# Kernel optimization log

Measured on AMD Instinct MI355X. Metric: run time of the kernel, lower is better.

The kernel has to match this reference:

```python
import jax, jax.numpy as jnp
import numpy as np

B, HID, REC, NC, T = 512, 196, 488, 35, 120
BN_EPS = 1e-3


def _bn(x, g, b):
    # eval-mode CustomBatchNorm1d: running_mean=0, running_var=1
    return g * (x / jnp.sqrt(1.0 + BN_EPS)) + b


def _gru(x, Wih, Whh, bih, bhh):
    """Standard torch nn.GRU (batch_first), h0 = 0. x: [B,T,D] -> [B,T,H]."""
    H = Whh.shape[1]
    def step(h, xt):
        xg = xt @ Wih.T + bih          # [B,3H]
        hg = h @ Whh.T + bhh           # [B,3H]
        xr, xz, xn = jnp.split(xg, 3, axis=1)
        hr, hz, hn = jnp.split(hg, 3, axis=1)
        r = jax.nn.sigmoid(xr + hr)
        z = jax.nn.sigmoid(xz + hz)
        n = jnp.tanh(xn + r * hn)
        h2 = (1.0 - z) * n + z * h
        return h2, h2
    h0 = jnp.zeros((x.shape[0], H), x.dtype)
    _, ys = jax.lax.scan(step, h0, jnp.swapaxes(x, 0, 1))
    return jnp.swapaxes(ys, 0, 1)


def _custom_gru(x, Wih, Whh, bih):
    """CustomGRUCell (eval mode: prev_target=0 so weight_tf term vanishes)."""
    H = Whh.shape[1]
    Whh_rz = Whh[:2 * H]
    Whh_n = Whh[2 * H:]
    b_r, b_z, b_n = bih[:H], bih[H:2 * H], bih[2 * H:]
    def step(h, xt):
        xg = xt @ Wih.T                 # [B,3H], no bias in F.linear
        xr, xz, xn = jnp.split(xg, 3, axis=1)
        hg = h @ Whh_rz.T               # only r,z rows needed (h_h chunk unused)
        hr, hz = jnp.split(hg, 2, axis=1)
        r = jax.nn.sigmoid(xr + hr + b_r)
        u = jax.nn.sigmoid(xz + hz + b_z)
        n = jax.nn.softmax(xn + (r * h) @ Whh_n.T + b_n, axis=1)
        h2 = (1.0 - u) * n + u * h
        return h2, h2
    h0 = jnp.zeros((x.shape[0], H), x.dtype)
    _, ys = jax.lax.scan(step, h0, jnp.swapaxes(x, 0, 1))
    return jnp.swapaxes(ys, 0, 1)


def setup_inputs() -> dict:
    key = jax.random.key(0)
    ks = jax.random.split(key, 16)
    s = 0.05
    inp = {
        "z_in": jax.random.normal(ks[0], (B, HID), jnp.float32),
        "W0": jax.random.normal(ks[1], (HID, HID), jnp.float32) * s,
        "b0": jnp.zeros((HID,), jnp.float32),
        "g0": jnp.full((1, HID), 0.1, jnp.float32),
        "beta0": jnp.zeros((1, HID), jnp.float32),
        "W1": jax.random.normal(ks[2], (HID, HID), jnp.float32) * s,
        "b1": jnp.zeros((HID,), jnp.float32),
        "g1": jnp.full((1, HID), 0.1, jnp.float32),
        "beta1": jnp.zeros((1, HID), jnp.float32),
        "gru0_Wih": jax.random.normal(ks[3], (3 * REC, HID), jnp.float32) * s,
        "gru0_Whh": jax.random.normal(ks[4], (3 * REC, REC), jnp.float32) * s,
        "gru0_bih": jax.random.normal(ks[5], (3 * REC,), jnp.float32) * s,
        "gru0_bhh": jax.random.normal(ks[6], (3 * REC,), jnp.float32) * s,
        "gru1_Wih": jax.random.normal(ks[7], (3 * REC, REC), jnp.float32) * s,
        "gru1_Whh": jax.random.normal(ks[8], (3 * REC, REC), jnp.float32) * s,
        "gru1_bih": jax.random.normal(ks[9], (3 * REC,), jnp.float32) * s,
        "gru1_bhh": jax.random.normal(ks[10], (3 * REC,), jnp.float32) * s,
        "cell_Wih": jax.random.normal(ks[11], (3 * NC, REC), jnp.float32) * s,
        "cell_Whh": jax.random.normal(ks[12], (3 * NC, NC), jnp.float32) * s,
        "cell_bih": jax.random.normal(ks[13], (3 * NC,), jnp.float32) * s,
    }
    return inp


def reference(z_in, W0, b0, g0, beta0, W1, b1, g1, beta1,
              gru0_Wih, gru0_Whh, gru0_bih, gru0_bhh,
              gru1_Wih, gru1_Whh, gru1_bih, gru1_bhh,
              cell_Wih, cell_Whh, cell_bih):
    z = _bn(z_in @ W0.T + b0, g0, beta0)
    z = _bn(z @ W1.T + b1, g1, beta1)
    z_reps = jnp.broadcast_to(z[:, None, :], (z.shape[0], T, z.shape[1]))
    x = _gru(z_reps, gru0_Wih, gru0_Whh, gru0_bih, gru0_bhh)
    x = _gru(x, gru1_Wih, gru1_Whh, gru1_bih, gru1_bhh)
    x_out = _custom_gru(x, cell_Wih, cell_Whh, cell_bih)  # [B,T,NCHARS]
    return x_out
```

## Files before the change

### kernel.cpp

```cpp
#include <hip/hip_runtime.h>
#include <math.h>

#define Bsz 512
#define HID 196
#define REC 488
#define NC  35
#define TT  120
#define G3  (3*REC)

#define KT   16
#define NT   31
#define AS   36
#define WS   36

struct GSmem   { float A[2][KT][AS]; float W[2][3][KT][WS]; };
struct CellSmem{ float xs[4][492]; float hs[4][40]; float rh[4][40]; };
union  PipeSmem{ GSmem g; CellSmem c; };

__device__ __forceinline__ float sigmoidf_(float x) { return 1.0f / (1.0f + __expf(-x)); }

__global__ void dense_bn_kernel(const float* __restrict__ X, const float* __restrict__ W,
                                const float* __restrict__ bias, const float* __restrict__ g,
                                const float* __restrict__ beta, float* __restrict__ Y) {
  __shared__ float xs[HID];
  int b = blockIdx.x;
  for (int k = threadIdx.x; k < HID; k += blockDim.x) xs[k] = X[(size_t)b*HID + k];
  __syncthreads();
  int j = threadIdx.x;
  if (j < HID) {
    const float4* wr = (const float4*)(W + (size_t)j*HID);
    float acc = 0.f;
    #pragma unroll 7
    for (int k4 = 0; k4 < HID/4; ++k4) {
      float4 w4 = wr[k4];
      acc += xs[4*k4+0]*w4.x + xs[4*k4+1]*w4.y + xs[4*k4+2]*w4.z + xs[4*k4+3]*w4.w;
    }
    float v = (acc + bias[j]) * 0.9995003746f;
    Y[(size_t)b*HID + j] = g[j]*v + beta[j];
  }
}

__global__ void xg0_kernel(const float* __restrict__ Z, const float* __restrict__ Wih,
                           const float* __restrict__ bih, float* __restrict__ XG) {
  __shared__ float zs[HID];
  int b = blockIdx.x;
  for (int k = threadIdx.x; k < HID; k += blockDim.x) zs[k] = Z[(size_t)b*HID + k];
  __syncthreads();
  for (int c = threadIdx.x; c < G3; c += blockDim.x) {
    const float4* wr = (const float4*)(Wih + (size_t)c*HID);
    float acc = 0.f;
    for (int k4 = 0; k4 < HID/4; ++k4) {
      float4 w4 = wr[k4];
      acc += zs[4*k4+0]*w4.x + zs[4*k4+1]*w4.y + zs[4*k4+2]*w4.z + zs[4*k4+3]*w4.w;
    }
    XG[(size_t)b*G3 + c] = acc + bih[c];
  }
}

__device__ __forceinline__ void loadA32(float (&dst)[KT][AS], const float* __restrict__ A,
                                        int b0, int kk) {
  int t = threadIdx.x;
  if (t < 128) {
    int row  = t >> 2;
    int kloc = (t & 3) << 2;
    int kb   = kk + kloc;
    float4 v = make_float4(0.f,0.f,0.f,0.f);
    if (kb + 3 < REC) v = *(const float4*)(A + (size_t)(b0 + row)*REC + kb);
    dst[kloc+0][row]=v.x; dst[kloc+1][row]=v.y; dst[kloc+2][row]=v.z; dst[kloc+3][row]=v.w;
  }
}

__device__ __forceinline__ void loadW3(float (&dst)[3][KT][WS], const float* __restrict__ W,
                                       int c0, int cvalid, int kk) {
  int t = threadIdx.x;
  #pragma unroll
  for (int s = 0; s < 2; ++s) {
    int idx = t + (s << 8);
    if (idx < 384) {
      int g    = idx >> 7;
      int rem  = idx & 127;
      int c    = rem >> 2;
      int kloc = (rem & 3) << 2;
      int kb   = kk + kloc;
      float4 v = make_float4(0.f,0.f,0.f,0.f);
      if (c < cvalid && kb + 3 < REC)
        v = *(const float4*)(W + (size_t)(g*REC + c0 + c)*REC + kb);
      dst[g][kloc+0][c]=v.x; dst[g][kloc+1][c]=v.y; dst[g][kloc+2][c]=v.z; dst[g][kloc+3][c]=v.w;
    }
  }
}

__device__ __forceinline__ void mma3(const float (&A)[KT][AS], const float (&W)[3][KT][WS],
                                     float (&ar)[2][2], float (&az)[2][2], float (&an)[2][2]) {
  int tx = threadIdx.x & 15, ty = threadIdx.x >> 4;
  #pragma unroll
  for (int k = 0; k < KT; ++k) {
    float a0 = A[k][ty*2 + 0];
    float a1 = A[k][ty*2 + 1];
    float wr0 = W[0][k][tx*2], wr1 = W[0][k][tx*2+1];
    float wz0 = W[1][k][tx*2], wz1 = W[1][k][tx*2+1];
    float wn0 = W[2][k][tx*2], wn1 = W[2][k][tx*2+1];
    ar[0][0]=fmaf(a0,wr0,ar[0][0]); ar[0][1]=fmaf(a0,wr1,ar[0][1]);
    ar[1][0]=fmaf(a1,wr0,ar[1][0]); ar[1][1]=fmaf(a1,wr1,ar[1][1]);
    az[0][0]=fmaf(a0,wz0,az[0][0]); az[0][1]=fmaf(a0,wz1,az[0][1]);
    az[1][0]=fmaf(a1,wz0,az[1][0]); az[1][1]=fmaf(a1,wz1,az[1][1]);
    an[0][0]=fmaf(a0,wn0,an[0][0]); an[0][1]=fmaf(a0,wn1,an[0][1]);
    an[1][0]=fmaf(a1,wn0,an[1][0]); an[1][1]=fmaf(a1,wn1,an[1][1]);
  }
}

__device__ __forceinline__ void gemm3_pass(GSmem& S, const float* __restrict__ A,
                                           const float* __restrict__ W,
                                           int b0, int c0, int cvalid,
                                           float (&ar)[2][2], float (&az)[2][2], float (&an)[2][2]) {
  loadA32(S.A[0], A, b0, 0);
  loadW3 (S.W[0], W, c0, cvalid, 0);
  __syncthreads();
  for (int tl = 0; tl < NT; ++tl) {
    int cur = tl & 1, nxt = cur ^ 1;
    if (tl + 1 < NT) {
      loadA32(S.A[nxt], A, b0, (tl+1)*KT);
      loadW3 (S.W[nxt], W, c0, cvalid, (tl+1)*KT);
    }
    mma3(S.A[cur], S.W[cur], ar, az, an);
    __syncthreads();
  }
}

__global__ __launch_bounds__(256)
void pipe_kernel(const float* __restrict__ xg0,
                 float* __restrict__ h0buf, float* __restrict__ h1buf, float* __restrict__ hcbuf,
                 float* __restrict__ out,
                 const float* __restrict__ Whh0, const float* __restrict__ bhh0,
                 const float* __restrict__ Wih1, const float* __restrict__ Whh1,
                 const float* __restrict__ bih1, const float* __restrict__ bhh1,
                 const float* __restrict__ cWih, const float* __restrict__ cWhh,
                 const float* __restrict__ cb, int s) {
  __shared__ PipeSmem S;
  int blk = blockIdx.x;

  if (blk < 256) {
    if (s >= TT) return;
    int rt = blk >> 4, ct = blk & 15;
    int b0 = rt << 5;
    int c0 = ct << 5;
    int cvalid = REC - c0; if (cvalid > 32) cvalid = 32;
    const float* hprev = h0buf + (size_t)((s+1)&1)*Bsz*REC;
    float*       hnew  = h0buf + (size_t)(s&1)*Bsz*REC;
    float ar[2][2]={{0}}, az[2][2]={{0}}, an[2][2]={{0}};
    gemm3_pass(S.g, hprev, Whh0, b0, c0, cvalid, ar, az, an);
    int tx = threadIdx.x & 15, ty = threadIdx.x >> 4;
    #pragma unroll
    for (int i = 0; i < 2; ++i) {
      int b = b0 + ty*2 + i;
      const float* xgrow = xg0   + (size_t)b*G3;
      const float* hprow = hprev + (size_t)b*REC;
      float*       hnrow = hnew  + (size_t)b*REC;
      #pragma unroll
      for (int j = 0; j < 2; ++j) {
        int cl = tx*2 + j;
        if (cl >= cvalid) continue;
        int c = c0 + cl;
        float r = sigmoidf_(xgrow[c]        + ar[i][j] + bhh0[c]);
        float z = sigmoidf_(xgrow[REC+c]    + az[i][j] + bhh0[REC+c]);
        float n = tanhf    (xgrow[2*REC+c]  + r*(an[i][j] + bhh0[2*REC+c]));
        hnrow[c] = (1.f - z)*n + z*hprow[c];
      }
    }
  } else if (blk < 512) {
    int t1 = s - 1;
    if (t1 < 0 || t1 >= TT) return;
    int bidx = blk - 256;
    int rt = bidx >> 4, ct = bidx & 15;
    int b0 = rt << 5;
    int c0 = ct << 5;
    int cvalid = REC - c0; if (cvalid > 32) cvalid = 32;
    const float* x     = h0buf + (size_t)(t1&1)*Bsz*REC;
    const float* hprev = h1buf + (size_t)((t1+1)&1)*Bsz*REC;
    float*       hnew  = h1buf + (size_t)(t1&1)*Bsz*REC;
    float ar[2][2]={{0}}, az[2][2]={{0}}, axn[2][2]={{0}}, ahn[2][2]={{0}};
    gemm3_pass(S.g, x,     Wih1, b0, c0, cvalid, ar, az, axn);
    gemm3_pass(S.g, hprev, Whh1, b0, c0, cvalid, ar, az, ahn);
    int tx = threadIdx.x & 15, ty = threadIdx.x >> 4;
    #pragma unroll
    for (int i = 0; i < 2; ++i) {
      int b = b0 + ty*2 + i;
      const float* hprow = hprev + (size_t)b*REC;
      float*       hnrow = hnew  + (size_t)b*REC;
      #pragma unroll
      for (int j = 0; j < 2; ++j) {
        int cl = tx*2 + j;
        if (cl >= cvalid) continue;
        int c = c0 + cl;
        float r = sigmoidf_(ar[i][j]  + bih1[c]       + bhh1[c]);
        float z = sigmoidf_(az[i][j]  + bih1[REC+c]   + bhh1[REC+c]);
        float n = tanhf    (axn[i][j] + bih1[2*REC+c] + r*(ahn[i][j] + bhh1[2*REC+c]));
        hnrow[c] = (1.f - z)*n + z*hprow[c];
      }
    }
  } else {
    int tc = s - 2;
    if (tc < 0) return;
    int ci = blk - 512;
    int wave = threadIdx.x >> 6;
    int lane = threadIdx.x & 63;
    int b = ci*4 + wave;
    const float* x  = h1buf + (size_t)(tc&1)*Bsz*REC;
    const float* hp = hcbuf + (size_t)((tc+1)&1)*Bsz*NC;
    float*       hn = hcbuf + (size_t)(tc&1)*Bsz*NC;
    float* xs = S.c.xs[wave];
    float* hs = S.c.hs[wave];
    float* rh = S.c.rh[wave];
    for (int k = lane; k < REC; k += 64) xs[k] = x[(size_t)b*REC + k];
    if (lane < NC) hs[lane] = hp[(size_t)b*NC + lane];
    __syncthreads();
    float v = -1e30f, u = 0.f, hpc = 0.f;
    if (lane < NC) {
      int c = lane;
      const float4* wr4 = (const float4*)(cWih + (size_t)c*REC);
      const float4* wz4 = (const float4*)(cWih + (size_t)(NC  + c)*REC);
      const float4* wn4 = (const float4*)(cWih + (size_t)(2*NC + c)*REC);
      float xr=0.f, xz=0.f, xn=0.f;
      #pragma unroll 2
      for (int k4 = 0; k4 < REC/4; ++k4) {
        float4 wa = wr4[k4], wb = wz4[k4], wc = wn4[k4];
        float x0=xs[4*k4], x1=xs[4*k4+1], x2=xs[4*k4+2], x3=xs[4*k4+3];
        xr += wa.x*x0 + wa.y*x1 + wa.z*x2 + wa.w*x3;
        xz += wb.x*x0 + wb.y*x1 + wb.z*x2 + wb.w*x3;
        xn += wc.x*x0 + wc.y*x1 + wc.z*x2 + wc.w*x3;
      }
      float hr=0.f, hz=0.f;
      for (int k = 0; k < NC; ++k) {
        float hv = hs[k];
        hr += hv * cWhh[(size_t)c*NC + k];
        hz += hv * cWhh[(size_t)(NC + c)*NC + k];
      }
      float r = sigmoidf_(xr + hr + cb[c]);
      u       = sigmoidf_(xz + hz + cb[NC + c]);
      hpc = hs[c];
      rh[c] = r * hpc;
      v = xn;
    }
    __syncthreads();
    if (lane < NC) {
      int c = lane;
      float hnn = 0.f;
      for (int k = 0; k < NC; ++k) hnn += rh[k] * cWhh[(size_t)(2*NC + c)*NC + k];
      v = v + hnn + cb[2*NC + c];
    }
    float m = v;
    #pragma unroll
    for (int o = 32; o > 0; o >>= 1) m = fmaxf(m, __shfl_xor(m, o));
    float e = (lane < NC) ? __expf(v - m) : 0.f;
    float ssum = e;
    #pragma unroll
    for (int o = 32; o > 0; o >>= 1) ssum += __shfl_xor(ssum, o);
    if (lane < NC) {
      float nsm = e / ssum;
      float h2 = (1.f - u)*nsm + u*hpc;
      hn[(size_t)b*NC + lane] = h2;
      out[((size_t)b*TT + tc)*NC + lane] = h2;
    }
  }
}

extern "C" void kernel_launch(void* const* d_in, const int* in_sizes, int n_in,
                              void* d_out, int out_size, void* d_ws, size_t ws_size,
                              hipStream_t stream) {
  const float* z_in  = (const float*)d_in[0];
  const float* W0    = (const float*)d_in[1];
  const float* b0    = (const float*)d_in[2];
  const float* g0    = (const float*)d_in[3];
  const float* beta0 = (const float*)d_in[4];
  const float* W1    = (const float*)d_in[5];
  const float* b1    = (const float*)d_in[6];
  const float* g1    = (const float*)d_in[7];
  const float* beta1 = (const float*)d_in[8];
  const float* Wih0  = (const float*)d_in[9];
  const float* Whh0  = (const float*)d_in[10];
  const float* bih0  = (const float*)d_in[11];
  const float* bhh0  = (const float*)d_in[12];
  const float* Wih1  = (const float*)d_in[13];
  const float* Whh1  = (const float*)d_in[14];
  const float* bih1  = (const float*)d_in[15];
  const float* bhh1  = (const float*)d_in[16];
  const float* cWih  = (const float*)d_in[17];
  const float* cWhh  = (const float*)d_in[18];
  const float* cbih  = (const float*)d_in[19];
  float* out = (float*)d_out;

  float* ws  = (float*)d_ws;
  float* z1  = ws;
  float* z2  = z1 + (size_t)Bsz*HID;
  float* xg0 = z2 + (size_t)Bsz*HID;
  float* h0  = xg0 + (size_t)Bsz*G3;
  float* h1  = h0 + 2*(size_t)Bsz*REC;
  float* hcb = h1 + 2*(size_t)Bsz*REC;
  size_t zero_floats = 2*(size_t)Bsz*REC * 2 + 2*(size_t)Bsz*NC;

  hipMemsetAsync(h0, 0, zero_floats * sizeof(float), stream);

  dense_bn_kernel<<<Bsz, 256, 0, stream>>>(z_in, W0, b0, g0, beta0, z1);
  dense_bn_kernel<<<Bsz, 256, 0, stream>>>(z1,   W1, b1, g1, beta1, z2);
  xg0_kernel     <<<Bsz, 256, 0, stream>>>(z2, Wih0, bih0, xg0);

  for (int s = 0; s < TT + 2; ++s) {
    pipe_kernel<<<640, 256, 0, stream>>>(xg0, h0, h1, hcb, out,
                                         Whh0, bhh0, Wih1, Whh1, bih1, bhh1,
                                         cWih, cWhh, cbih, s);
  }
}
```

Measured before the change: 13.16 ms.

## Replace per-step launches with persistent pipelined kernel using grid barriers

Replaces the 122 per-timestep kernel launches with a single persistent kernel of 247 blocks that syncs each pipeline slot through an atomic grid barrier. Layer-1 GRU is split into a separate input-projection stage and a recurrent stage, giving four pipelined stages. Hidden states are stored transposed, weights are pre-transposed into a k-major layout, and each block covers all 512 batch rows for 24 gate columns. The xg0 projection is also batched four rows per block. This removes launch overhead and improves weight reuse, but it depends on all blocks being co-resident (deadlock risk) and adds spin-barrier latency on every step.

```diff
diff --git a/kernel.cpp b/kernel.cpp
--- a/kernel.cpp
+++ b/kernel.cpp
@@ -6,18 +6,32 @@
 #define REC 488
 #define NC  35
 #define TT  120
-#define G3  (3*REC)
-
-#define KT   16
-#define NT   31
-#define AS   36
-#define WS   36
-
-struct GSmem   { float A[2][KT][AS]; float W[2][3][KT][WS]; };
-struct CellSmem{ float xs[4][492]; float hs[4][40]; float rh[4][40]; };
-union  PipeSmem{ GSmem g; CellSmem c; };
+#define G3  1464
+#define NSLOT 123
+
+#define KT   8
+#define NCH  61
+#define NB   61
+#define CBLK 64
+#define NGRID (3*NB + CBLK)
+
+union SU {
+  float a[2*KT*512];
+  struct { float xs[8][REC]; float hs[8][36]; float rh[8][36]; } c;
+};
 
 __device__ __forceinline__ float sigmoidf_(float x) { return 1.0f / (1.0f + __expf(-x)); }
+
+__device__ __forceinline__ void gbar(int* bar, int target) {
+  __syncthreads();
+  if (threadIdx.x == 0) {
+    __threadfence();
+    atomicAdd(bar, 1);
+    while (atomicAdd(bar, 0) < target) __builtin_amdgcn_s_sleep(8);
+    __threadfence();
+  }
+  __syncthreads();
+}
 
 __global__ void dense_bn_kernel(const float* __restrict__ X, const float* __restrict__ W,
                                 const float* __restrict__ bias, const float* __restrict__ g,
@@ -40,227 +54,261 @@
   }
 }
 
-__global__ void xg0_kernel(const float* __restrict__ Z, const float* __restrict__ Wih,
-                           const float* __restrict__ bih, float* __restrict__ XG) {
-  __shared__ float zs[HID];
-  int b = blockIdx.x;
-  for (int k = threadIdx.x; k < HID; k += blockDim.x) zs[k] = Z[(size_t)b*HID + k];
-  __syncthreads();
-  for (int c = threadIdx.x; c < G3; c += blockDim.x) {
+__global__ __launch_bounds__(256)
+void xg0v2_kernel(const float* __restrict__ Z, const float* __restrict__ Wih,
+                  const float* __restrict__ bih, float* __restrict__ XG) {
+  __shared__ float zs[HID*4];
+  int b0 = blockIdx.x << 2;
+  for (int idx = threadIdx.x; idx < HID*4; idx += 256) {
+    int k = idx >> 2, i = idx & 3;
+    zs[idx] = Z[(size_t)(b0+i)*HID + k];
+  }
+  __syncthreads();
+  for (int c = threadIdx.x; c < G3; c += 256) {
     const float4* wr = (const float4*)(Wih + (size_t)c*HID);
-    float acc = 0.f;
+    float a0=0.f,a1=0.f,a2=0.f,a3=0.f;
     for (int k4 = 0; k4 < HID/4; ++k4) {
-      float4 w4 = wr[k4];
-      acc += zs[4*k4+0]*w4.x + zs[4*k4+1]*w4.y + zs[4*k4+2]*w4.z + zs[4*k4+3]*w4.w;
-    }
-    XG[(size_t)b*G3 + c] = acc + bih[c];
-  }
-}
-
-__device__ __forceinline__ void loadA32(float (&dst)[KT][AS], const float* __restrict__ A,
-                                        int b0, int kk) {
-  int t = threadIdx.x;
-  if (t < 128) {
-    int row  = t >> 2;
-    int kloc = (t & 3) << 2;
-    int kb   = kk + kloc;
-    float4 v = make_float4(0.f,0.f,0.f,0.f);
-    if (kb + 3 < REC) v = *(const float4*)(A + (size_t)(b0 + row)*REC + kb);
-    dst[kloc+0][row]=v.x; dst[kloc+1][row]=v.y; dst[kloc+2][row]=v.z; dst[kloc+3][row]=v.w;
-  }
-}
-
-__device__ __forceinline__ void loadW3(float (&dst)[3][KT][WS], const float* __restrict__ W,
-                                       int c0, int cvalid, int kk) {
-  int t = threadIdx.x;
-  #pragma unroll
-  for (int s = 0; s < 2; ++s) {
-    int idx = t + (s << 8);
-    if (idx < 384) {
-      int g    = idx >> 7;
-      int rem  = idx & 127;
-      int c    = rem >> 2;
-      int kloc = (rem & 3) << 2;
-      int kb   = kk + kloc;
-      float4 v = make_float4(0.f,0.f,0.f,0.f);
-      if (c < cvalid && kb + 3 < REC)
-        v = *(const float4*)(W + (size_t)(g*REC + c0 + c)*REC + kb);
-      dst[g][kloc+0][c]=v.x; dst[g][kloc+1][c]=v.y; dst[g][kloc+2][c]=v.z; dst[g][kloc+3][c]=v.w;
-    }
-  }
-}
-
-__device__ __forceinline__ void mma3(const float (&A)[KT][AS], const float (&W)[3][KT][WS],
-                                     float (&ar)[2][2], float (&az)[2][2], float (&an)[2][2]) {
-  int tx = threadIdx.x & 15, ty = threadIdx.x >> 4;
-  #pragma unroll
-  for (int k = 0; k < KT; ++k) {
-    float a0 = A[k][ty*2 + 0];
-    float a1 = A[k][ty*2 + 1];
-    float wr0 = W[0][k][tx*2], wr1 = W[0][k][tx*2+1];
-    float wz0 = W[1][k][tx*2], wz1 = W[1][k][tx*2+1];
-    float wn0 = W[2][k][tx*2], wn1 = W[2][k][tx*2+1];
-    ar[0][0]=fmaf(a0,wr0,ar[0][0]); ar[0][1]=fmaf(a0,wr1,ar[0][1]);
-    ar[1][0]=fmaf(a1,wr0,ar[1][0]); ar[1][1]=fmaf(a1,wr1,ar[1][1]);
-    az[0][0]=fmaf(a0,wz0,az[0][0]); az[0][1]=fmaf(a0,wz1,az[0][1]);
-    az[1][0]=fmaf(a1,wz0,az[1][0]); az[1][1]=fmaf(a1,wz1,az[1][1]);
-    an[0][0]=fmaf(a0,wn0,an[0][0]); an[0][1]=fmaf(a0,wn1,an[0][1]);
-    an[1][0]=fmaf(a1,wn0,an[1][0]); an[1][1]=fmaf(a1,wn1,an[1][1]);
-  }
-}
-
-__device__ __forceinline__ void gemm3_pass(GSmem& S, const float* __restrict__ A,
-                                           const float* __restrict__ W,
-                                           int b0, int c0, int cvalid,
-                                           float (&ar)[2][2], float (&az)[2][2], float (&an)[2][2]) {
-  loadA32(S.A[0], A, b0, 0);
-  loadW3 (S.W[0], W, c0, cvalid, 0);
-  __syncthreads();
-  for (int tl = 0; tl < NT; ++tl) {
-    int cur = tl & 1, nxt = cur ^ 1;
-    if (tl + 1 < NT) {
-      loadA32(S.A[nxt], A, b0, (tl+1)*KT);
-      loadW3 (S.W[nxt], W, c0, cvalid, (tl+1)*KT);
-    }
-    mma3(S.A[cur], S.W[cur], ar, az, an);
+      float4 w = wr[k4];
+      const float* zp = zs + (k4<<4);
+      a0=fmaf(w.x,zp[0],a0);  a1=fmaf(w.x,zp[1],a1);  a2=fmaf(w.x,zp[2],a2);  a3=fmaf(w.x,zp[3],a3);
+      a0=fmaf(w.y,zp[4],a0);  a1=fmaf(w.y,zp[5],a1);  a2=fmaf(w.y,zp[6],a2);  a3=fmaf(w.y,zp[7],a3);
+      a0=fmaf(w.z,zp[8],a0);  a1=fmaf(w.z,zp[9],a1);  a2=fmaf(w.z,zp[10],a2); a3=fmaf(w.z,zp[11],a3);
+      a0=fmaf(w.w,zp[12],a0); a1=fmaf(w.w,zp[13],a1); a2=fmaf(w.w,zp[14],a2); a3=fmaf(w.w,zp[15],a3);
+    }
+    float bb = bih[c];
+    XG[(size_t)(b0+0)*G3 + c] = a0 + bb;
+    XG[(size_t)(b0+1)*G3 + c] = a1 + bb;
+    XG[(size_t)(b0+2)*G3 + c] = a2 + bb;
+    XG[(size_t)(b0+3)*G3 + c] = a3 + bb;
+  }
+}
+
+__global__ __launch_bounds__(256)
+void wtrans_kernel(const float* __restrict__ Whh0, const float* __restrict__ Wih1,
+                   const float* __restrict__ Whh1, float* __restrict__ Wt) {
+  int blk = blockIdx.x;
+  int stage = blk / NB, j = blk - stage*NB;
+  const float* Wsrc = (stage==0) ? Whh0 : (stage==1) ? Wih1 : Whh1;
+  float* dst = Wt + (size_t)stage*REC*G3;
+  for (int idx = threadIdx.x; idx < 24*REC; idx += 256) {
+    int r = idx / REC, k = idx - r*REC;
+    int g = r >> 3, cl = r & 7;
+    dst[(size_t)k*G3 + j*24 + r] = Wsrc[(size_t)(g*REC + j*8 + cl)*REC + k];
+  }
+}
+
+__device__ __forceinline__ void gemm24(const float* __restrict__ AslabT,
+                                       const float* __restrict__ Wt, int j,
+                                       float* lds, float (&acc)[48])
+{
+  const int tid = threadIdx.x;
+  const int l = tid & 63, w = tid >> 6;
+  const int rb = (w << 7) + l;
+  float4 hold[4];
+  {
+    const float4* gsrc = (const float4*)AslabT;
+    #pragma unroll
+    for (int i = 0; i < 4; ++i) hold[i] = gsrc[tid + (i<<8)];
+    float4* d = (float4*)lds;
+    #pragma unroll
+    for (int i = 0; i < 4; ++i) d[tid + (i<<8)] = hold[i];
+  }
+  __syncthreads();
+  for (int ck = 0; ck < NCH; ++ck) {
+    if (ck + 1 < NCH) {
+      const float4* gsrc = (const float4*)(AslabT + (size_t)(ck+1)*(KT*512));
+      #pragma unroll
+      for (int i = 0; i < 4; ++i) hold[i] = gsrc[tid + (i<<8)];
+    }
+    const float* As = lds + (ck & 1)*(KT*512);
+    const float* Wk = Wt + (size_t)ck*KT*G3 + j*24;
+    #pragma unroll
+    for (int k = 0; k < KT; ++k) {
+      float a0 = As[k*512 + rb];
+      float a1 = As[k*512 + rb + 64];
+      const float* wk = Wk + (size_t)k*G3;
+      #pragma unroll
+      for (int r = 0; r < 24; ++r) {
+        float wv = wk[r];
+        acc[r*2+0] = fmaf(a0, wv, acc[r*2+0]);
+        acc[r*2+1] = fmaf(a1, wv, acc[r*2+1]);
+      }
+    }
+    if (ck + 1 < NCH) {
+      float4* d = (float4*)(lds + ((ck+1)&1)*(KT*512));
+      #pragma unroll
+      for (int i = 0; i < 4; ++i) d[tid + (i<<8)] = hold[i];
+    }
     __syncthreads();
   }
 }
 
 __global__ __launch_bounds__(256)
-void pipe_kernel(const float* __restrict__ xg0,
-                 float* __restrict__ h0buf, float* __restrict__ h1buf, float* __restrict__ hcbuf,
-                 float* __restrict__ out,
-                 const float* __restrict__ Whh0, const float* __restrict__ bhh0,
-                 const float* __restrict__ Wih1, const float* __restrict__ Whh1,
+void pers_kernel(const float* __restrict__ xg0,
+                 float* __restrict__ h0T, float* __restrict__ h1T,
+                 float* __restrict__ h1N, float* __restrict__ xg1,
+                 float* __restrict__ hc, float* __restrict__ out,
+                 const float* __restrict__ Wt,
+                 const float* __restrict__ bhh0,
                  const float* __restrict__ bih1, const float* __restrict__ bhh1,
                  const float* __restrict__ cWih, const float* __restrict__ cWhh,
-                 const float* __restrict__ cb, int s) {
-  __shared__ PipeSmem S;
-  int blk = blockIdx.x;
-
-  if (blk < 256) {
-    if (s >= TT) return;
-    int rt = blk >> 4, ct = blk & 15;
-    int b0 = rt << 5;
-    int c0 = ct << 5;
-    int cvalid = REC - c0; if (cvalid > 32) cvalid = 32;
-    const float* hprev = h0buf + (size_t)((s+1)&1)*Bsz*REC;
-    float*       hnew  = h0buf + (size_t)(s&1)*Bsz*REC;
-    float ar[2][2]={{0}}, az[2][2]={{0}}, an[2][2]={{0}};
-    gemm3_pass(S.g, hprev, Whh0, b0, c0, cvalid, ar, az, an);
-    int tx = threadIdx.x & 15, ty = threadIdx.x >> 4;
-    #pragma unroll
-    for (int i = 0; i < 2; ++i) {
-      int b = b0 + ty*2 + i;
-      const float* xgrow = xg0   + (size_t)b*G3;
-      const float* hprow = hprev + (size_t)b*REC;
-      float*       hnrow = hnew  + (size_t)b*REC;
-      #pragma unroll
-      for (int j = 0; j < 2; ++j) {
-        int cl = tx*2 + j;
-        if (cl >= cvalid) continue;
-        int c = c0 + cl;
-        float r = sigmoidf_(xgrow[c]        + ar[i][j] + bhh0[c]);
-        float z = sigmoidf_(xgrow[REC+c]    + az[i][j] + bhh0[REC+c]);
-        float n = tanhf    (xgrow[2*REC+c]  + r*(an[i][j] + bhh0[2*REC+c]));
-        hnrow[c] = (1.f - z)*n + z*hprow[c];
-      }
-    }
-  } else if (blk < 512) {
-    int t1 = s - 1;
-    if (t1 < 0 || t1 >= TT) return;
-    int bidx = blk - 256;
-    int rt = bidx >> 4, ct = bidx & 15;
-    int b0 = rt << 5;
-    int c0 = ct << 5;
-    int cvalid = REC - c0; if (cvalid > 32) cvalid = 32;
-    const float* x     = h0buf + (size_t)(t1&1)*Bsz*REC;
-    const float* hprev = h1buf + (size_t)((t1+1)&1)*Bsz*REC;
-    float*       hnew  = h1buf + (size_t)(t1&1)*Bsz*REC;
-    float ar[2][2]={{0}}, az[2][2]={{0}}, axn[2][2]={{0}}, ahn[2][2]={{0}};
-    gemm3_pass(S.g, x,     Wih1, b0, c0, cvalid, ar, az, axn);
-    gemm3_pass(S.g, hprev, Whh1, b0, c0, cvalid, ar, az, ahn);
-    int tx = threadIdx.x & 15, ty = threadIdx.x >> 4;
-    #pragma unroll
-    for (int i = 0; i < 2; ++i) {
-      int b = b0 + ty*2 + i;
-      const float* hprow = hprev + (size_t)b*REC;
-      float*       hnrow = hnew  + (size_t)b*REC;
-      #pragma unroll
-      for (int j = 0; j < 2; ++j) {
-        int cl = tx*2 + j;
-        if (cl >= cvalid) continue;
-        int c = c0 + cl;
-        float r = sigmoidf_(ar[i][j]  + bih1[c]       + bhh1[c]);
-        float z = sigmoidf_(az[i][j]  + bih1[REC+c]   + bhh1[REC+c]);
-        float n = tanhf    (axn[i][j] + bih1[2*REC+c] + r*(ahn[i][j] + bhh1[2*REC+c]));
-        hnrow[c] = (1.f - z)*n + z*hprow[c];
-      }
-    }
-  } else {
-    int tc = s - 2;
-    if (tc < 0) return;
-    int ci = blk - 512;
-    int wave = threadIdx.x >> 6;
-    int lane = threadIdx.x & 63;
-    int b = ci*4 + wave;
-    const float* x  = h1buf + (size_t)(tc&1)*Bsz*REC;
-    const float* hp = hcbuf + (size_t)((tc+1)&1)*Bsz*NC;
-    float*       hn = hcbuf + (size_t)(tc&1)*Bsz*NC;
-    float* xs = S.c.xs[wave];
-    float* hs = S.c.hs[wave];
-    float* rh = S.c.rh[wave];
-    for (int k = lane; k < REC; k += 64) xs[k] = x[(size_t)b*REC + k];
-    if (lane < NC) hs[lane] = hp[(size_t)b*NC + lane];
-    __syncthreads();
-    float v = -1e30f, u = 0.f, hpc = 0.f;
-    if (lane < NC) {
-      int c = lane;
-      const float4* wr4 = (const float4*)(cWih + (size_t)c*REC);
-      const float4* wz4 = (const float4*)(cWih + (size_t)(NC  + c)*REC);
-      const float4* wn4 = (const float4*)(cWih + (size_t)(2*NC + c)*REC);
-      float xr=0.f, xz=0.f, xn=0.f;
-      #pragma unroll 2
-      for (int k4 = 0; k4 < REC/4; ++k4) {
-        float4 wa = wr4[k4], wb = wz4[k4], wc = wn4[k4];
-        float x0=xs[4*k4], x1=xs[4*k4+1], x2=xs[4*k4+2], x3=xs[4*k4+3];
-        xr += wa.x*x0 + wa.y*x1 + wa.z*x2 + wa.w*x3;
-        xz += wb.x*x0 + wb.y*x1 + wb.z*x2 + wb.w*x3;
-        xn += wc.x*x0 + wc.y*x1 + wc.z*x2 + wc.w*x3;
-      }
-      float hr=0.f, hz=0.f;
-      for (int k = 0; k < NC; ++k) {
-        float hv = hs[k];
-        hr += hv * cWhh[(size_t)c*NC + k];
-        hz += hv * cWhh[(size_t)(NC + c)*NC + k];
-      }
-      float r = sigmoidf_(xr + hr + cb[c]);
-      u       = sigmoidf_(xz + hz + cb[NC + c]);
-      hpc = hs[c];
-      rh[c] = r * hpc;
-      v = xn;
-    }
-    __syncthreads();
-    if (lane < NC) {
-      int c = lane;
-      float hnn = 0.f;
-      for (int k = 0; k < NC; ++k) hnn += rh[k] * cWhh[(size_t)(2*NC + c)*NC + k];
-      v = v + hnn + cb[2*NC + c];
-    }
-    float m = v;
-    #pragma unroll
-    for (int o = 32; o > 0; o >>= 1) m = fmaxf(m, __shfl_xor(m, o));
-    float e = (lane < NC) ? __expf(v - m) : 0.f;
-    float ssum = e;
-    #pragma unroll
-    for (int o = 32; o > 0; o >>= 1) ssum += __shfl_xor(ssum, o);
-    if (lane < NC) {
-      float nsm = e / ssum;
-      float h2 = (1.f - u)*nsm + u*hpc;
-      hn[(size_t)b*NC + lane] = h2;
-      out[((size_t)b*TT + tc)*NC + lane] = h2;
-    }
+                 const float* __restrict__ cb, int* __restrict__ bar)
+{
+  __shared__ SU S;
+  const int blk = blockIdx.x;
+  const int tid = threadIdx.x;
+  const int stage = (blk < NB) ? 0 : (blk < 2*NB) ? 1 : (blk < 3*NB) ? 2 : 3;
+  const int l = tid & 63, w = tid >> 6;
+  const int rb = (w << 7) + l;
+
+  for (int s = 0; s < NSLOT; ++s) {
+    if (stage == 0) {
+      if (s < TT) {
+        int j = blk;
+        const float* hprevT = h0T + (size_t)((s+1)&1)*REC*Bsz;
+        float*       hnewT  = h0T + (size_t)(s&1)*REC*Bsz;
+        float acc[48] = {0};
+        gemm24(hprevT, Wt, j, S.a, acc);
+        int c0 = j*8;
+        #pragma unroll
+        for (int cl = 0; cl < 8; ++cl) {
+          int c = c0 + cl;
+          float br = bhh0[c], bz = bhh0[REC+c], bn = bhh0[2*REC+c];
+          #pragma unroll
+          for (int i = 0; i < 2; ++i) {
+            int b = rb + (i<<6);
+            const float* xr = xg0 + (size_t)b*G3;
+            float r = sigmoidf_(xr[c]       + acc[cl*2+i]        + br);
+            float z = sigmoidf_(xr[REC+c]   + acc[(8+cl)*2+i]    + bz);
+            float n = tanhf   (xr[2*REC+c] + r*(acc[(16+cl)*2+i] + bn));
+            hnewT[(size_t)c*Bsz + b] = (1.f-z)*n + z*hprevT[(size_t)c*Bsz + b];
+          }
+        }
+      }
+    } else if (stage == 1) {
+      if (s >= 1 && s <= TT) {
+        int j = blk - NB;
+        int t1 = s - 1;
+        const float* xT  = h0T + (size_t)(t1&1)*REC*Bsz;
+        float*       xgw = xg1 + (size_t)(t1&1)*Bsz*G3;
+        float acc[48] = {0};
+        gemm24(xT, Wt + (size_t)REC*G3, j, S.a, acc);
+        int c0 = j*8;
+        #pragma unroll
+        for (int cl = 0; cl < 8; ++cl) {
+          int c = c0 + cl;
+          #pragma unroll
+          for (int i = 0; i < 2; ++i) {
+            int b = rb + (i<<6);
+            float* o = xgw + (size_t)b*G3;
+            o[c]         = acc[cl*2+i];
+            o[REC+c]     = acc[(8+cl)*2+i];
+            o[2*REC+c]   = acc[(16+cl)*2+i];
+          }
+        }
+      }
+    } else if (stage == 2) {
+      if (s >= 2 && s <= TT+1) {
+        int j = blk - 2*NB;
+        int t2 = s - 2;
+        const float* hprevT = h1T + (size_t)((t2+1)&1)*REC*Bsz;
+        float*       hnewT  = h1T + (size_t)(t2&1)*REC*Bsz;
+        float*       hnewN  = h1N + (size_t)(t2&1)*Bsz*REC;
+        const float* xgr    = xg1 + (size_t)(t2&1)*Bsz*G3;
+        float acc[48] = {0};
+        gemm24(hprevT, Wt + 2*(size_t)REC*G3, j, S.a, acc);
+        int c0 = j*8;
+        #pragma unroll
+        for (int cl = 0; cl < 8; ++cl) {
+          int c = c0 + cl;
+          float br = bih1[c] + bhh1[c];
+          float bz = bih1[REC+c] + bhh1[REC+c];
+          float bnx = bih1[2*REC+c], bnh = bhh1[2*REC+c];
+          #pragma unroll
+          for (int i = 0; i < 2; ++i) {
+            int b = rb + (i<<6);
+            const float* xr = xgr + (size_t)b*G3;
+            float r = sigmoidf_(xr[c]       + acc[cl*2+i]     + br);
+            float z = sigmoidf_(xr[REC+c]   + acc[(8+cl)*2+i] + bz);
+            float n = tanhf   (xr[2*REC+c] + bnx + r*(acc[(16+cl)*2+i] + bnh));
+            float h2 = (1.f-z)*n + z*hprevT[(size_t)c*Bsz + b];
+            hnewT[(size_t)c*Bsz + b] = h2;
+            hnewN[(size_t)b*REC + c] = h2;
+          }
+        }
+      }
+    } else {
+      if (s >= 3) {
+        int t3 = s - 3;
+        int b0 = (blk - 3*NB) << 3;
+        const float* x  = h1N + (size_t)(t3&1)*Bsz*REC;
+        const float* hp = hc  + (size_t)((t3+1)&1)*Bsz*NC;
+        float*       hn = hc  + (size_t)(t3&1)*Bsz*NC;
+        for (int it = 0; it < 8; ++it)
+          for (int k = tid; k < REC; k += 256)
+            S.c.xs[it][k] = x[(size_t)(b0+it)*REC + k];
+        if (l < NC) {
+          #pragma unroll
+          for (int q = 0; q < 2; ++q) {
+            int it = (w<<1) + q;
+            S.c.hs[it][l] = hp[(size_t)(b0+it)*NC + l];
+          }
+        }
+        __syncthreads();
+        for (int q = 0; q < 2; ++q) {
+          int it = (w<<1) + q;
+          int b = b0 + it;
+          float v = -1e30f, u = 0.f, hpc = 0.f;
+          if (l < NC) {
+            const float4* wr4 = (const float4*)(cWih + (size_t)l*REC);
+            const float4* wz4 = (const float4*)(cWih + (size_t)(NC+l)*REC);
+            const float4* wn4 = (const float4*)(cWih + (size_t)(2*NC+l)*REC);
+            const float4* xs4 = (const float4*)(S.c.xs[it]);
+            float xr=0.f, xz=0.f, xn=0.f;
+            #pragma unroll 2
+            for (int k4 = 0; k4 < REC/4; ++k4) {
+              float4 xv = xs4[k4];
+              float4 wa = wr4[k4], wb = wz4[k4], wc = wn4[k4];
+              xr += wa.x*xv.x + wa.y*xv.y + wa.z*xv.z + wa.w*xv.w;
+              xz += wb.x*xv.x + wb.y*xv.y + wb.z*xv.z + wb.w*xv.w;
+              xn += wc.x*xv.x + wc.y*xv.y + wc.z*xv.z + wc.w*xv.w;
+            }
+            float hr=0.f, hz=0.f;
+            for (int k = 0; k < NC; ++k) {
+              float hv = S.c.hs[it][k];
+              hr = fmaf(hv, cWhh[(size_t)l*NC + k], hr);
+              hz = fmaf(hv, cWhh[(size_t)(NC+l)*NC + k], hz);
+            }
+            float r = sigmoidf_(xr + hr + cb[l]);
+            u       = sigmoidf_(xz + hz + cb[NC+l]);
+            hpc = S.c.hs[it][l];
+            S.c.rh[it][l] = r * hpc;
+            v = xn;
+          }
+          __syncthreads();
+          if (l < NC) {
+            float hnn = 0.f;
+            for (int k = 0; k < NC; ++k)
+              hnn = fmaf(S.c.rh[it][k], cWhh[(size_t)(2*NC+l)*NC + k], hnn);
+            v = v + hnn + cb[2*NC+l];
+          }
+          float m = v;
+          #pragma unroll
+          for (int o = 32; o; o >>= 1) m = fmaxf(m, __shfl_xor(m, o));
+          float e = (l < NC) ? __expf(v - m) : 0.f;
+          float ss = e;
+          #pragma unroll
+          for (int o = 32; o; o >>= 1) ss += __shfl_xor(ss, o);
+          if (l < NC) {
+            float h2 = (1.f - u)*(e/ss) + u*hpc;
+            hn[(size_t)b*NC + l] = h2;
+            out[((size_t)b*TT + t3)*NC + l] = h2;
+          }
+        }
+        __syncthreads();
+      }
+    }
+    gbar(bar, NGRID*(s+1));
   }
 }
 
@@ -290,23 +338,25 @@
   float* out = (float*)d_out;
 
   float* ws  = (float*)d_ws;
-  float* z1  = ws;
-  float* z2  = z1 + (size_t)Bsz*HID;
-  float* xg0 = z2 + (size_t)Bsz*HID;
-  float* h0  = xg0 + (size_t)Bsz*G3;
-  float* h1  = h0 + 2*(size_t)Bsz*REC;
-  float* hcb = h1 + 2*(size_t)Bsz*REC;
-  size_t zero_floats = 2*(size_t)Bsz*REC * 2 + 2*(size_t)Bsz*NC;
-
-  hipMemsetAsync(h0, 0, zero_floats * sizeof(float), stream);
+  int*   bar = (int*)ws;
+  float* h0T = ws  + 256;
+  float* h1T = h0T + 2*(size_t)REC*Bsz;
+  float* hcb = h1T + 2*(size_t)REC*Bsz;
+  float* h1N = hcb + 2*(size_t)Bsz*NC;
+  float* xg1 = h1N + 2*(size_t)Bsz*REC;
+  float* xg0 = xg1 + 2*(size_t)Bsz*G3;
+  float* z1  = xg0 + (size_t)Bsz*G3;
+  float* z2  = z1  + (size_t)Bsz*HID;
+  float* Wt  = z2  + (size_t)Bsz*HID;
+
+  size_t zero_floats = 256 + 4*(size_t)REC*Bsz + 2*(size_t)Bsz*NC;
+  hipMemsetAsync(ws, 0, zero_floats*sizeof(float), stream);
 
   dense_bn_kernel<<<Bsz, 256, 0, stream>>>(z_in, W0, b0, g0, beta0, z1);
   dense_bn_kernel<<<Bsz, 256, 0, stream>>>(z1,   W1, b1, g1, beta1, z2);
-  xg0_kernel     <<<Bsz, 256, 0, stream>>>(z2, Wih0, bih0, xg0);
-
-  for (int s = 0; s < TT + 2; ++s) {
-    pipe_kernel<<<640, 256, 0, stream>>>(xg0, h0, h1, hcb, out,
-                                         Whh0, bhh0, Wih1, Whh1, bih1, bhh1,
-                                         cWih, cWhh, cbih, s);
-  }
-}
+  xg0v2_kernel   <<<128, 256, 0, stream>>>(z2, Wih0, bih0, xg0);
+  wtrans_kernel  <<<3*NB, 256, 0, stream>>>(Whh0, Wih1, Whh1, Wt);
+
+  pers_kernel<<<NGRID, 256, 0, stream>>>(xg0, h0T, h1T, h1N, xg1, hcb, out,
+                                         Wt, bhh0, bih1, bhh1, cWih, cWhh, cbih, bar);
+}
```

After: 39.46 ms. 200% more time.
